# Kernel tuning notes

Measured on AMD Instinct MI355X. Metric: run time of the kernel, lower is better.

## Reference

```python
import jax, jax.numpy as jnp
import numpy as np

N_HEAD = 16
N_KV_HEAD = 4
N_EMBD = 2048
HEAD_DIM = N_EMBD // N_HEAD  # 128
RMS_EPS = float(np.finfo(np.float32).eps)  # torch F.rms_norm default eps


def _apply_rotary(x, cos, sin):
    # x: [B,T,H,D]; cos/sin: [1,T,1,D/2]
    d = x.shape[-1] // 2
    x1, x2 = x[..., :d], x[..., d:]
    y1 = x1 * cos + x2 * sin
    y2 = -x1 * sin + x2 * cos
    return jnp.concatenate([y1, y2], axis=-1)


def _rms_norm(x):
    var = jnp.mean(jnp.square(x), axis=-1, keepdims=True)
    return x * jax.lax.rsqrt(var + RMS_EPS)


def setup_inputs() -> dict:
    key = jax.random.key(0)
    ks = jax.random.split(key, 7)
    B, T = 2, 2048
    x = jax.random.normal(ks[0], (B, T, N_EMBD), dtype=jnp.float32)
    cos = jax.random.normal(ks[1], (1, T, 1, HEAD_DIM // 2), dtype=jnp.float32)
    sin = jax.random.normal(ks[2], (1, T, 1, HEAD_DIM // 2), dtype=jnp.float32)
    s = 1.0 / np.sqrt(N_EMBD)
    Wq = jax.random.normal(ks[3], (N_HEAD * HEAD_DIM, N_EMBD), dtype=jnp.float32) * s
    Wk = jax.random.normal(ks[4], (N_KV_HEAD * HEAD_DIM, N_EMBD), dtype=jnp.float32) * s
    Wv = jax.random.normal(ks[5], (N_KV_HEAD * HEAD_DIM, N_EMBD), dtype=jnp.float32) * s
    Wo = jax.random.normal(ks[6], (N_EMBD, N_EMBD), dtype=jnp.float32) * s
    return {"x": x, "cos": cos, "sin": sin, "Wq": Wq, "Wk": Wk, "Wv": Wv, "Wo": Wo}


def reference(x, cos, sin, Wq, Wk, Wv, Wo):
    B, T, C = x.shape
    q = (x @ Wq.T).reshape(B, T, N_HEAD, HEAD_DIM)
    k = (x @ Wk.T).reshape(B, T, N_KV_HEAD, HEAD_DIM)
    v = (x @ Wv.T).reshape(B, T, N_KV_HEAD, HEAD_DIM)
    q = _rms_norm(_apply_rotary(q, cos, sin))
    k = _rms_norm(_apply_rotary(k, cos, sin))
    # to [B,H,T,D]; expand kv heads for GQA
    q = q.transpose(0, 2, 1, 3)
    k = k.transpose(0, 2, 1, 3)
    v = v.transpose(0, 2, 1, 3)
    g = N_HEAD // N_KV_HEAD
    k = jnp.repeat(k, g, axis=1)
    v = jnp.repeat(v, g, axis=1)
    scale = 1.0 / np.sqrt(HEAD_DIM)
    scores = jnp.einsum("bhtd,bhsd->bhts", q, k) * scale
    causal = jnp.tril(jnp.ones((T, T), dtype=bool))
    scores = jnp.where(causal, scores, -jnp.inf)
    attn = jax.nn.softmax(scores, axis=-1)
    y = jnp.einsum("bhts,bhsd->bhtd", attn, v)
    y = y.transpose(0, 2, 1, 3).reshape(B, T, C)
    return y @ Wo.T
```

## Files before the change

kernel.cpp:

```cpp
#include <hip/hip_runtime.h>
#include <hip/hip_bf16.h>
#include <stdint.h>

#define B_   2
#define T_   2048
#define CEMB 2048
#define H_   16
#define HKV_ 4
#define D_   128

typedef __attribute__((ext_vector_type(8))) short bf16x8;
typedef __attribute__((ext_vector_type(4))) float f32x4;
typedef __attribute__((ext_vector_type(16))) float f32x16;

#if __has_builtin(__builtin_amdgcn_exp2f)
#define EXP2(x) __builtin_amdgcn_exp2f(x)
#else
#define EXP2(x) exp2f(x)
#endif

__device__ __forceinline__ unsigned short f2b(float f) {
  union { float f; unsigned u; } v; v.f = f;
  unsigned r = v.u + 0x7FFFu + ((v.u >> 16) & 1u);
  return (unsigned short)(r >> 16);
}
__device__ __forceinline__ float b2f(unsigned short u) {
  union { unsigned u; float f; } v; v.u = ((unsigned)u) << 16; return v.f;
}
__device__ __forceinline__ unsigned cvtpk(float lo, float hi) {
  unsigned r;
  asm("v_cvt_pk_bf16_f32 %0, %1, %2" : "=v"(r) : "v"(lo), "v"(hi));
  return r;
}

#if __has_builtin(__builtin_amdgcn_permlane32_swap)
__device__ __forceinline__ void pl32(unsigned& a, unsigned& b) {
  auto r = __builtin_amdgcn_permlane32_swap(a, b, false, false);
  a = r[0]; b = r[1];
}
#else
__device__ __forceinline__ void pl32(unsigned& a, unsigned& b) {
  const bool hih = (threadIdx.x & 32) != 0;
  unsigned sa = __shfl_xor(a, 32), sb = __shfl_xor(b, 32);
  unsigned na = hih ? sb : a;
  unsigned nb = hih ? b : sa;
  a = na; b = nb;
}
#endif

__device__ __forceinline__ void gl16(const void* g, void* l) {
  __builtin_amdgcn_global_load_lds(
      (const __attribute__((address_space(1))) unsigned int*)g,
      (__attribute__((address_space(3))) unsigned int*)l, 16, 0, 0);
}

#define FENCE() asm volatile("" ::: "memory")

__global__ void cvt_kernel(const float* __restrict__ src,
                           unsigned short* __restrict__ dst, int n4) {
  int i = blockIdx.x * blockDim.x + threadIdx.x;
  const int stride = gridDim.x * blockDim.x;
  for (; i < n4; i += stride) {
    float4 v = ((const float4*)src)[i];
    ushort4 o;
    o.x = f2b(v.x); o.y = f2b(v.y); o.z = f2b(v.z); o.w = f2b(v.w);
    ((ushort4*)dst)[i] = o;
  }
}

__global__ __launch_bounds__(512, 2)
void gemm_n192(const unsigned short* __restrict__ A,
               const unsigned short* __restrict__ W,
               unsigned short* __restrict__ Cmat, int M, int N, int K) {
  __shared__ alignas(16) unsigned short As[2][2][128][64];
  __shared__ alignas(16) unsigned short Bs[2][192][64];

  const int tid  = threadIdx.x;
  const int lane = tid & 63;
  const int w    = tid >> 6;
  const int wr   = w >> 2;
  const int wc   = w & 3;
  const int l16  = lane & 15, g4 = lane >> 4;
  const int srow = lane >> 3;
  const int schk = lane & 7;

  const int gx  = gridDim.x;
  const int nwg = gx * gridDim.y;
  const int lin = blockIdx.y * gx + blockIdx.x;
  const int cpx = nwg >> 3;
  const int swz = (lin & 7) * cpx + (lin >> 3);
  const int m0 = (swz / gx) * 256;
  const int n0 = (swz % gx) * 192;

  const unsigned short* Ap = A + (size_t)m0 * K;
  const unsigned short* Wp = W + (size_t)n0 * K;
  const int nk = K >> 6;

  f32x4 acc[8][3] = {};

  auto stA = [&](int ts, int h) {
    const unsigned short* g = Ap + (size_t)(h * 128 + w * 8 + srow) * K
                                 + ts * 64 + ((schk ^ srow) << 3);
    unsigned short* l = &As[ts & 1][h][w * 8][0];
    gl16(g, l);
    gl16(g + (size_t)64 * K, l + 64 * 64);
  };
  auto stB = [&](int ts, int j) {
    const unsigned short* g = Wp + (size_t)(j * 64 + w * 8 + srow) * K
                                 + ts * 64 + ((schk ^ srow) << 3);
    gl16(g, &Bs[ts & 1][j * 64 + w * 8][0]);
  };

  stA(0, 0); stA(0, 1); stB(0, 0); stB(0, 1); stB(0, 2);
  stA(1, 0); stB(1, 0); stB(1, 1); stB(1, 2);
  asm volatile("s_waitcnt vmcnt(5)" ::: "memory");
  __builtin_amdgcn_s_barrier();
  FENCE();

  for (int t = 0; t < nk; ++t) {
    const int buf = t & 1;
    bf16x8 af[4][2], bfr[3][2];
    #pragma unroll
    for (int mi = 0; mi < 4; ++mi) {
      const int har = (mi * 2 + wr) * 16 + l16;
      #pragma unroll
      for (int ks = 0; ks < 2; ++ks)
        af[mi][ks] = *(const bf16x8*)&As[buf][0][har][((ks * 4 + g4) ^ (l16 & 7)) << 3];
    }
    #pragma unroll
    for (int fc = 0; fc < 3; ++fc) {
      const int br = wc * 48 + fc * 16 + l16;
      #pragma unroll
      for (int ks = 0; ks < 2; ++ks)
        bfr[fc][ks] = *(const bf16x8*)&Bs[buf][br][((ks * 4 + g4) ^ (l16 & 7)) << 3];
    }
    if (t + 1 < nk) stA(t + 1, 1);
    __builtin_amdgcn_s_setprio(1);
    #pragma unroll
    for (int mi = 0; mi < 4; ++mi) {
      #pragma unroll
      for (int fc = 0; fc < 3; ++fc) {
        f32x4 a = acc[mi][fc];
        a = __builtin_amdgcn_mfma_f32_16x16x32_bf16(af[mi][0], bfr[fc][0], a, 0, 0, 0);
        a = __builtin_amdgcn_mfma_f32_16x16x32_bf16(af[mi][1], bfr[fc][1], a, 0, 0, 0);
        acc[mi][fc] = a;
      }
    }
    __builtin_amdgcn_s_setprio(0);
    if (t + 2 < nk) asm volatile("s_waitcnt vmcnt(7)" ::: "memory");
    else            asm volatile("s_waitcnt vmcnt(0)" ::: "memory");
    __builtin_amdgcn_s_barrier();
    FENCE();
    #pragma unroll
    for (int mi = 0; mi < 4; ++mi) {
      const int har = (mi * 2 + wr) * 16 + l16;
      #pragma unroll
      for (int ks = 0; ks < 2; ++ks)
        af[mi][ks] = *(const bf16x8*)&As[buf][1][har][((ks * 4 + g4) ^ (l16 & 7)) << 3];
    }
    if (t + 2 < nk) { stA(t + 2, 0); stB(t + 2, 0); stB(t + 2, 1); stB(t + 2, 2); }
    __builtin_amdgcn_s_setprio(1);
    #pragma unroll
    for (int mi = 0; mi < 4; ++mi) {
      #pragma unroll
      for (int fc = 0; fc < 3; ++fc) {
        f32x4 a = acc[4 + mi][fc];
        a = __builtin_amdgcn_mfma_f32_16x16x32_bf16(af[mi][0], bfr[fc][0], a, 0, 0, 0);
        a = __builtin_amdgcn_mfma_f32_16x16x32_bf16(af[mi][1], bfr[fc][1], a, 0, 0, 0);
        acc[4 + mi][fc] = a;
      }
    }
    __builtin_amdgcn_s_setprio(0);
    if (t + 2 < nk) asm volatile("s_waitcnt vmcnt(7)" ::: "memory");
    else            asm volatile("s_waitcnt vmcnt(0)" ::: "memory");
    __builtin_amdgcn_s_barrier();
    FENCE();
  }

  #pragma unroll
  for (int fr = 0; fr < 8; ++fr) {
    const int hh = fr >> 2, mi = fr & 3;
    #pragma unroll
    for (int fc = 0; fc < 3; ++fc) {
      const int row = m0 + hh * 128 + (mi * 2 + wr) * 16 + g4 * 4;
      const int col = n0 + wc * 48 + fc * 16 + l16;
      #pragma unroll
      for (int r = 0; r < 4; ++r)
        Cmat[(size_t)(row + r) * N + col] = f2b(acc[fr][fc][r]);
    }
  }
}

__global__ __launch_bounds__(512, 2)
void gemm_n128(const unsigned short* __restrict__ A,
               const unsigned short* __restrict__ W,
               float* __restrict__ Cmat, int M, int N, int K) {
  __shared__ alignas(16) unsigned short As[2][2][128][64];
  __shared__ alignas(16) unsigned short Bs[2][2][64][64];

  const int tid  = threadIdx.x;
  const int lane = tid & 63;
  const int w    = tid >> 6;
  const int wr   = w >> 2;
  const int wc   = w & 3;
  const int l16  = lane & 15, g4 = lane >> 4;
  const int srow = lane >> 3;
  const int schk = lane & 7;

  const int gx  = gridDim.x;
  const int nwg = gx * gridDim.y;
  const int lin = blockIdx.y * gx + blockIdx.x;
  const int cpx = nwg >> 3;
  const int swz = (lin & 7) * cpx + (lin >> 3);
  const int m0 = (swz / gx) * 256;
  const int n0 = (swz % gx) * 128;

  const unsigned short* Ap = A + (size_t)m0 * K;
  const unsigned short* Wp = W + (size_t)n0 * K;
  const int nk = K >> 6;

  const int bh_ = wc >> 1;
  const int br0 = (wc & 1) * 32;

  f32x4 acc[8][2] = {};

  auto stA = [&](int ts, int h) {
    const unsigned short* g = Ap + (size_t)(h * 128 + w * 8 + srow) * K
                                 + ts * 64 + ((schk ^ srow) << 3);
    unsigned short* l = &As[ts & 1][h][w * 8][0];
    gl16(g, l);
    gl16(g + (size_t)64 * K, l + 64 * 64);
  };
  auto stB = [&](int ts, int h) {
    const unsigned short* g = Wp + (size_t)(h * 64 + w * 8 + srow) * K
                                 + ts * 64 + ((schk ^ srow) << 3);
    gl16(g, &Bs[ts & 1][h][w * 8][0]);
  };

  stA(0, 0); stA(0, 1); stB(0, 0); stB(0, 1);
  stA(1, 0); stB(1, 0); stB(1, 1);
  asm volatile("s_waitcnt vmcnt(4)" ::: "memory");
  __builtin_amdgcn_s_barrier();
  FENCE();

  for (int t = 0; t < nk; ++t) {
    const int buf = t & 1;
    bf16x8 af[4][2], bfr[2][2];
    #pragma unroll
    for (int mi = 0; mi < 4; ++mi) {
      const int har = (mi * 2 + wr) * 16 + l16;
      #pragma unroll
      for (int ks = 0; ks < 2; ++ks)
        af[mi][ks] = *(const bf16x8*)&As[buf][0][har][((ks * 4 + g4) ^ (l16 & 7)) << 3];
    }
    #pragma unroll
    for (int fc = 0; fc < 2; ++fc) {
      const int br = br0 + fc * 16 + l16;
      #pragma unroll
      for (int ks = 0; ks < 2; ++ks)
        bfr[fc][ks] = *(const bf16x8*)&Bs[buf][bh_][br][((ks * 4 + g4) ^ (l16 & 7)) << 3];
    }
    if (t + 1 < nk) stA(t + 1, 1);
    __builtin_amdgcn_s_setprio(1);
    #pragma unroll
    for (int mi = 0; mi < 4; ++mi) {
      #pragma unroll
      for (int fc = 0; fc < 2; ++fc) {
        f32x4 a = acc[mi][fc];
        a = __builtin_amdgcn_mfma_f32_16x16x32_bf16(af[mi][0], bfr[fc][0], a, 0, 0, 0);
        a = __builtin_amdgcn_mfma_f32_16x16x32_bf16(af[mi][1], bfr[fc][1], a, 0, 0, 0);
        acc[mi][fc] = a;
      }
    }
    __builtin_amdgcn_s_setprio(0);
    if (t + 2 < nk) asm volatile("s_waitcnt vmcnt(6)" ::: "memory");
    else            asm volatile("s_waitcnt vmcnt(0)" ::: "memory");
    __builtin_amdgcn_s_barrier();
    FENCE();
    #pragma unroll
    for (int mi = 0; mi < 4; ++mi) {
      const int har = (mi * 2 + wr) * 16 + l16;
      #pragma unroll
      for (int ks = 0; ks < 2; ++ks)
        af[mi][ks] = *(const bf16x8*)&As[buf][1][har][((ks * 4 + g4) ^ (l16 & 7)) << 3];
    }
    if (t + 2 < nk) { stA(t + 2, 0); stB(t + 2, 0); stB(t + 2, 1); }
    __builtin_amdgcn_s_setprio(1);
    #pragma unroll
    for (int mi = 0; mi < 4; ++mi) {
      #pragma unroll
      for (int fc = 0; fc < 2; ++fc) {
        f32x4 a = acc[4 + mi][fc];
        a = __builtin_amdgcn_mfma_f32_16x16x32_bf16(af[mi][0], bfr[fc][0], a, 0, 0, 0);
        a = __builtin_amdgcn_mfma_f32_16x16x32_bf16(af[mi][1], bfr[fc][1], a, 0, 0, 0);
        acc[4 + mi][fc] = a;
      }
    }
    __builtin_amdgcn_s_setprio(0);
    if (t + 2 < nk) asm volatile("s_waitcnt vmcnt(6)" ::: "memory");
    else            asm volatile("s_waitcnt vmcnt(0)" ::: "memory");
    __builtin_amdgcn_s_barrier();
    FENCE();
  }

  #pragma unroll
  for (int fr = 0; fr < 8; ++fr) {
    const int hh = fr >> 2, mi = fr & 3;
    #pragma unroll
    for (int fc = 0; fc < 2; ++fc) {
      const int row = m0 + hh * 128 + (mi * 2 + wr) * 16 + g4 * 4;
      const int col = n0 + wc * 32 + fc * 16 + l16;
      #pragma unroll
      for (int r = 0; r < 4; ++r)
        Cmat[(size_t)(row + r) * N + col] = acc[fr][fc][r];
    }
  }
}

__global__ __launch_bounds__(128)
void rope_norm(const unsigned short* __restrict__ X, int rstride,
               const float* __restrict__ Cos, const float* __restrict__ Sin,
               unsigned short* __restrict__ Out, int Hn, float out_scale) {
  const int idx = blockIdx.x;
  const int h  = idx % Hn;
  const int bt = idx / Hn;
  const int t  = bt & (T_ - 1);
  const int b  = bt >> 11;
  const int d  = threadIdx.x;
  const unsigned short* src = X + (size_t)bt * rstride + h * D_;
  float y;
  if (d < 64) {
    float x1 = b2f(src[d]), x2 = b2f(src[d + 64]);
    float c = Cos[t * 64 + d], s = Sin[t * 64 + d];
    y = x1 * c + x2 * s;
  } else {
    int dd = d - 64;
    float x1 = b2f(src[dd]), x2 = b2f(src[d]);
    float c = Cos[t * 64 + dd], s = Sin[t * 64 + dd];
    y = -x1 * s + x2 * c;
  }
  float ss = y * y;
  #pragma unroll
  for (int m = 32; m; m >>= 1) ss += __shfl_xor(ss, m);
  __shared__ float red[2];
  if ((d & 63) == 0) red[d >> 6] = ss;
  __syncthreads();
  const float tot  = red[0] + red[1];
  const float rinv = rsqrtf(tot * (1.0f / 128.0f) + 1.1920929e-7f) * out_scale;
  Out[(((size_t)b * Hn + h) * T_ + t) * D_ + d] = f2b(y * rinv);
}

__global__ __launch_bounds__(256)
void vtrans(const unsigned short* __restrict__ Vf, int rstride,
            unsigned short* __restrict__ Vt) {
  __shared__ float tile[32][65];
  const int t0 = blockIdx.x * 64;
  const int d0 = blockIdx.y * 32;
  const int bh = blockIdx.z;
  const int b = bh >> 2, hk = bh & 3;
  const int tid = threadIdx.x;
  {
    const int di = tid & 31, ts = tid >> 5;
    #pragma unroll
    for (int i = 0; i < 8; ++i) {
      int tt = ts + i * 8;
      tile[di][tt] = b2f(Vf[(size_t)(b * T_ + t0 + tt) * rstride + hk * D_ + d0 + di]);
    }
  }
  __syncthreads();
  {
    const int ti = tid & 63, ds = tid >> 6;
    #pragma unroll
    for (int i = 0; i < 8; ++i) {
      int dd = ds * 8 + i;
      Vt[((size_t)bh * D_ + d0 + dd) * T_ + t0 + ti] = f2b(tile[dd][ti]);
    }
  }
}

#define KVB 128

__global__ __launch_bounds__(512)
void attn_kernel(const unsigned short* __restrict__ Qn,
                 const unsigned short* __restrict__ Kn,
                 const unsigned short* __restrict__ Vt,
                 unsigned short* __restrict__ Yb) {
  __shared__ alignas(16) unsigned short Ks[2][KVB][D_];
  __shared__ alignas(16) unsigned short Vs[2][D_][KVB];

  const int tid = threadIdx.x;
  const int lane = tid & 63;
  const int w = tid >> 6;
  const int wq  = w & 3;
  const int kvg = w >> 2;
  const int l31 = lane & 31;
  const int hi  = lane >> 5;
  const int bh = blockIdx.x;
  const int by = blockIdx.y;
  const int qt = (by < 8) ? by : 23 - by;
  const int b = bh >> 4, h = bh & 15;
  const int hk = h >> 2;

  const unsigned short* kp = Kn + ((size_t)(b * HKV_ + hk) * T_) * D_;
  const unsigned short* vp = Vt + ((size_t)(b * HKV_ + hk) * D_) * T_;

  const int r4 = lane >> 4, c16 = lane & 15;

  const int t0 = qt * 128;
  const int qrow0 = t0 + wq * 32;
  const int qmax = qrow0 + 31;
  const int nt = qt + 1;
  const int qglob = qrow0 + l31;

  const unsigned short* qp = Qn + ((size_t)bh * T_ + qrow0) * D_;
  bf16x8 qf[8];
  #pragma unroll
  for (int ds = 0; ds < 8; ++ds)
    qf[ds] = *(const bf16x8*)(qp + (size_t)l31 * D_ + ds * 16 + hi * 8);

  f32x16 o[4] = {};
  float l_lane = 0.f;

  auto stage = [&](int tt) {
    const int buf = tt & 1;
    const int kv = tt * KVB;
    #pragma unroll
    for (int j = 0; j < 4; ++j) {
      const int row = w * 16 + j * 4 + r4;
      const int cg = c16 ^ (row & 7);
      gl16(kp + (size_t)(kv + row) * D_ + cg * 8, &Ks[buf][w * 16 + j * 4][0]);
    }
    #pragma unroll
    for (int j = 0; j < 4; ++j) {
      const int row = w * 16 + j * 4 + r4;
      const int cg = c16 ^ (row & 7);
      gl16(vp + (size_t)row * T_ + kv + cg * 8, &Vs[buf][w * 16 + j * 4][0]);
    }
  };

  stage(0);

  union PAu { unsigned u[4]; bf16x8 v; };

  for (int t = 0; t < nt; ++t) {
    __syncthreads();
    if (t + 1 < nt) stage(t + 1);
    const int kbase = t * KVB + kvg * 64;
    if (kbase <= qmax) {
      const unsigned short (*kb)[D_]  = Ks[t & 1];
      const unsigned short (*vbp)[KVB] = Vs[t & 1];
      f32x16 s0 = {}, s1 = {};
      __builtin_amdgcn_s_setprio(1);
      #pragma unroll
      for (int ds = 0; ds < 8; ++ds) {
        const int key0 = kvg * 64 + l31;
        const int key1 = kvg * 64 + 32 + l31;
        bf16x8 k0 = *(const bf16x8*)&kb[key0][(((ds * 2 + hi) ^ (key0 & 7)) << 3)];
        bf16x8 k1 = *(const bf16x8*)&kb[key1][(((ds * 2 + hi) ^ (key1 & 7)) << 3)];
        s0 = __builtin_amdgcn_mfma_f32_32x32x16_bf16(k0, qf[ds], s0, 0, 0, 0);
        s1 = __builtin_amdgcn_mfma_f32_32x32x16_bf16(k1, qf[ds], s1, 0, 0, 0);
      }
      __builtin_amdgcn_s_setprio(0);
      const bool need_mask = (kbase + 63 > qrow0);
      float e0[16], e1[16];
      float ls = 0.f;
      #pragma unroll
      for (int r = 0; r < 16; ++r) {
        const int crow = (r & 3) + 8 * (r >> 2) + 4 * hi;
        float v0 = EXP2(s0[r]);
        float v1 = EXP2(s1[r]);
        if (need_mask) {
          v0 = (kbase + crow      <= qglob) ? v0 : 0.f;
          v1 = (kbase + 32 + crow <= qglob) ? v1 : 0.f;
        }
        e0[r] = v0; e1[r] = v1;
        ls += v0 + v1;
      }
      l_lane += ls;
      PAu pa[4];
      {
        unsigned a0 = cvtpk(e0[0],  e0[1]),  a1 = cvtpk(e0[2],  e0[3]);
        unsigned b0 = cvtpk(e0[4],  e0[5]),  b1 = cvtpk(e0[6],  e0[7]);
        unsigned c0 = cvtpk(e0[8],  e0[9]),  c1 = cvtpk(e0[10], e0[11]);
        unsigned d0 = cvtpk(e0[12], e0[13]), d1 = cvtpk(e0[14], e0[15]);
        pl32(a0, b0); pl32(a1, b1); pl32(c0, d0); pl32(c1, d1);
        pa[0].u[0] = a0; pa[0].u[1] = a1; pa[0].u[2] = b0; pa[0].u[3] = b1;
        pa[1].u[0] = c0; pa[1].u[1] = c1; pa[1].u[2] = d0; pa[1].u[3] = d1;
      }
      {
        unsigned a0 = cvtpk(e1[0],  e1[1]),  a1 = cvtpk(e1[2],  e1[3]);
        unsigned b0 = cvtpk(e1[4],  e1[5]),  b1 = cvtpk(e1[6],  e1[7]);
        unsigned c0 = cvtpk(e1[8],  e1[9]),  c1 = cvtpk(e1[10], e1[11]);
        unsigned d0 = cvtpk(e1[12], e1[13]), d1 = cvtpk(e1[14], e1[15]);
        pl32(a0, b0); pl32(a1, b1); pl32(c0, d0); pl32(c1, d1);
        pa[2].u[0] = a0; pa[2].u[1] = a1; pa[2].u[2] = b0; pa[2].u[3] = b1;
        pa[3].u[0] = c0; pa[3].u[1] = c1; pa[3].u[2] = d0; pa[3].u[3] = d1;
      }
      __builtin_amdgcn_s_setprio(1);
      #pragma unroll
      for (int ks = 0; ks < 4; ++ks) {
        #pragma unroll
        for (int db = 0; db < 4; ++db) {
          const int d = db * 32 + l31;
          const int c = (kvg * 8 + ks * 2 + hi) ^ (d & 7);
          bf16x8 vf = *(const bf16x8*)&vbp[d][c << 3];
          o[db] = __builtin_amdgcn_mfma_f32_32x32x16_bf16(pa[ks].v, vf, o[db], 0, 0, 0);
        }
      }
      __builtin_amdgcn_s_setprio(0);
    }
  }

  const float lfull = l_lane + __shfl_xor(l_lane, 32);
  __syncthreads();
  float* obuf = (float*)&Ks[0][0][0];
  float* lbuf = (float*)&Vs[0][0][0];
  if (w >= 4) {
    const int base = (w - 4) * 4096;
    #pragma unroll
    for (int r = 0; r < 16; ++r)
      #pragma unroll
      for (int db = 0; db < 4; ++db)
        obuf[base + (r * 4 + db) * 64 + lane] = o[db][r];
    if (hi == 0) lbuf[(w - 4) * 32 + l31] = lfull;
  }
  __syncthreads();
  if (w < 4) {
    const int base = w * 4096;
    const float ltot = lfull + lbuf[w * 32 + l31];
    const float invq = 1.0f / ltot;
    #pragma unroll
    for (int r = 0; r < 16; ++r) {
      const int crow = (r & 3) + 8 * (r >> 2) + 4 * hi;
      const float inv = __shfl(invq, crow);
      unsigned short* yrow = Yb + ((size_t)(b * T_ + qrow0 + crow) * CEMB) + h * D_;
      #pragma unroll
      for (int db = 0; db < 4; ++db)
        yrow[db * 32 + l31] = f2b((o[db][r] + obuf[base + (r * 4 + db) * 64 + lane]) * inv);
    }
  }
}

extern "C" void kernel_launch(void* const* d_in, const int* in_sizes, int n_in,
                              void* d_out, int out_size, void* d_ws, size_t ws_size,
                              hipStream_t stream) {
  const float* x    = (const float*)d_in[0];
  const float* cosp = (const float*)d_in[1];
  const float* sinp = (const float*)d_in[2];
  const float* Wq   = (const float*)d_in[3];
  const float* Wk   = (const float*)d_in[4];
  const float* Wv   = (const float*)d_in[5];
  const float* Wo   = (const float*)d_in[6];
  float* out = (float*)d_out;

  char* ws = (char*)d_ws;
  size_t off = 0;
  auto alloc = [&](size_t bytes) {
    void* p = ws + off;
    off += (bytes + 255) & ~(size_t)255;
    return p;
  };
  const size_t MT = (size_t)B_ * T_;
  const int NQKV = 3072;
  unsigned short* xb    = (unsigned short*)alloc(MT * CEMB * 2);
  unsigned short* wqkvb = (unsigned short*)alloc((size_t)NQKV * 2048 * 2);
  unsigned short* wob   = (unsigned short*)alloc((size_t)2048 * 2048 * 2);
  unsigned short* qkvb  = (unsigned short*)alloc(MT * NQKV * 2);
  unsigned short* qn    = (unsigned short*)alloc((size_t)B_ * H_ * T_ * D_ * 2);
  unsigned short* kn    = (unsigned short*)alloc((size_t)B_ * HKV_ * T_ * D_ * 2);
  unsigned short* vt    = (unsigned short*)alloc((size_t)B_ * HKV_ * D_ * T_ * 2);
  unsigned short* yb    = (unsigned short*)alloc(MT * CEMB * 2);

  cvt_kernel<<<2048, 256, 0, stream>>>(x,  xb, (int)(MT * CEMB / 4));
  cvt_kernel<<<1024, 256, 0, stream>>>(Wq, wqkvb,                2048 * 2048 / 4);
  cvt_kernel<<<256,  256, 0, stream>>>(Wk, wqkvb + 2048 * 2048,  512 * 2048 / 4);
  cvt_kernel<<<256,  256, 0, stream>>>(Wv, wqkvb + 2560 * 2048,  512 * 2048 / 4);
  cvt_kernel<<<1024, 256, 0, stream>>>(Wo, wob,                  2048 * 2048 / 4);

  gemm_n192<<<dim3(NQKV / 192, 4096 / 256), 512, 0, stream>>>(xb, wqkvb, qkvb, 4096, NQKV, 2048);

  rope_norm<<<4096 * H_,   128, 0, stream>>>(qkvb,        NQKV, cosp, sinp, qn, H_,   0.1275174324f);
  rope_norm<<<4096 * HKV_, 128, 0, stream>>>(qkvb + 2048, NQKV, cosp, sinp, kn, HKV_, 1.0f);
  vtrans<<<dim3(T_ / 64, D_ / 32, B_ * HKV_), 256, 0, stream>>>(qkvb + 2560, NQKV, vt);

  attn_kernel<<<dim3(B_ * H_, 16), 512, 0, stream>>>(qn, kn, vt, yb);

  gemm_n128<<<dim3(2048 / 128, 4096 / 256), 512, 0, stream>>>(yb, wob, out, 4096, 2048, 2048);
}
```

Baseline: 197.1 us.

## Retile GEMM warps to 4x2 grid, simplify pipeline, widen attention LDS swizzle

Both GEMM kernels change their wave layout from 2x4 to 4x2. Each wave now covers a 64-row by 96- or 64-column sub-tile and runs a single half-step per K-tile instead of two halves. This cuts per-wave LDS fragment loads for A, but the K-tile prefetch now issues all loads for the next stage at once and waits with vmcnt(0) every iteration, which may expose memory latency. The attention kernel's K/V shared-memory XOR swizzle widens from 8 to 16 chunks to reduce bank conflicts on the 128-wide rows.

Result: no change. 195.6 us (-0.7%).

```diff
diff --git a/kernel.cpp b/kernel.cpp
--- a/kernel.cpp
+++ b/kernel.cpp
@@ -78,8 +78,8 @@
   const int tid  = threadIdx.x;
   const int lane = tid & 63;
   const int w    = tid >> 6;
-  const int wr   = w >> 2;
-  const int wc   = w & 3;
+  const int wm   = w >> 1;
+  const int wn   = w & 1;
   const int l16  = lane & 15, g4 = lane >> 4;
   const int srow = lane >> 3;
   const int schk = lane & 7;
@@ -96,7 +96,10 @@
   const unsigned short* Wp = W + (size_t)n0 * K;
   const int nk = K >> 6;
 
-  f32x4 acc[8][3] = {};
+  const int hA  = wm >> 1;
+  const int ra0 = (wm & 1) * 64;
+
+  f32x4 acc[4][6] = {};
 
   auto stA = [&](int ts, int h) {
     const unsigned short* g = Ap + (size_t)(h * 128 + w * 8 + srow) * K
@@ -112,34 +115,36 @@
   };
 
   stA(0, 0); stA(0, 1); stB(0, 0); stB(0, 1); stB(0, 2);
-  stA(1, 0); stB(1, 0); stB(1, 1); stB(1, 2);
-  asm volatile("s_waitcnt vmcnt(5)" ::: "memory");
+  asm volatile("s_waitcnt vmcnt(0)" ::: "memory");
   __builtin_amdgcn_s_barrier();
   FENCE();
 
   for (int t = 0; t < nk; ++t) {
     const int buf = t & 1;
-    bf16x8 af[4][2], bfr[3][2];
+    bf16x8 af[4][2], bfr[6][2];
     #pragma unroll
     for (int mi = 0; mi < 4; ++mi) {
-      const int har = (mi * 2 + wr) * 16 + l16;
+      const int ar = ra0 + mi * 16 + l16;
       #pragma unroll
       for (int ks = 0; ks < 2; ++ks)
-        af[mi][ks] = *(const bf16x8*)&As[buf][0][har][((ks * 4 + g4) ^ (l16 & 7)) << 3];
-    }
-    #pragma unroll
-    for (int fc = 0; fc < 3; ++fc) {
-      const int br = wc * 48 + fc * 16 + l16;
+        af[mi][ks] = *(const bf16x8*)&As[buf][hA][ar][((ks * 4 + g4) ^ (l16 & 7)) << 3];
+    }
+    #pragma unroll
+    for (int fc = 0; fc < 6; ++fc) {
+      const int br = wn * 96 + fc * 16 + l16;
       #pragma unroll
       for (int ks = 0; ks < 2; ++ks)
         bfr[fc][ks] = *(const bf16x8*)&Bs[buf][br][((ks * 4 + g4) ^ (l16 & 7)) << 3];
     }
-    if (t + 1 < nk) stA(t + 1, 1);
+    if (t + 1 < nk) {
+      stA(t + 1, 0); stA(t + 1, 1);
+      stB(t + 1, 0); stB(t + 1, 1); stB(t + 1, 2);
+    }
     __builtin_amdgcn_s_setprio(1);
     #pragma unroll
     for (int mi = 0; mi < 4; ++mi) {
       #pragma unroll
-      for (int fc = 0; fc < 3; ++fc) {
+      for (int fc = 0; fc < 6; ++fc) {
         f32x4 a = acc[mi][fc];
         a = __builtin_amdgcn_mfma_f32_16x16x32_bf16(af[mi][0], bfr[fc][0], a, 0, 0, 0);
         a = __builtin_amdgcn_mfma_f32_16x16x32_bf16(af[mi][1], bfr[fc][1], a, 0, 0, 0);
@@ -147,46 +152,20 @@
       }
     }
     __builtin_amdgcn_s_setprio(0);
-    if (t + 2 < nk) asm volatile("s_waitcnt vmcnt(7)" ::: "memory");
-    else            asm volatile("s_waitcnt vmcnt(0)" ::: "memory");
+    asm volatile("s_waitcnt vmcnt(0)" ::: "memory");
     __builtin_amdgcn_s_barrier();
     FENCE();
-    #pragma unroll
-    for (int mi = 0; mi < 4; ++mi) {
-      const int har = (mi * 2 + wr) * 16 + l16;
-      #pragma unroll
-      for (int ks = 0; ks < 2; ++ks)
-        af[mi][ks] = *(const bf16x8*)&As[buf][1][har][((ks * 4 + g4) ^ (l16 & 7)) << 3];
-    }
-    if (t + 2 < nk) { stA(t + 2, 0); stB(t + 2, 0); stB(t + 2, 1); stB(t + 2, 2); }
-    __builtin_amdgcn_s_setprio(1);
-    #pragma unroll
-    for (int mi = 0; mi < 4; ++mi) {
-      #pragma unroll
-      for (int fc = 0; fc < 3; ++fc) {
-        f32x4 a = acc[4 + mi][fc];
-        a = __builtin_amdgcn_mfma_f32_16x16x32_bf16(af[mi][0], bfr[fc][0], a, 0, 0, 0);
-        a = __builtin_amdgcn_mfma_f32_16x16x32_bf16(af[mi][1], bfr[fc][1], a, 0, 0, 0);
-        acc[4 + mi][fc] = a;
-      }
-    }
-    __builtin_amdgcn_s_setprio(0);
-    if (t + 2 < nk) asm volatile("s_waitcnt vmcnt(7)" ::: "memory");
-    else            asm volatile("s_waitcnt vmcnt(0)" ::: "memory");
-    __builtin_amdgcn_s_barrier();
-    FENCE();
   }
 
   #pragma unroll
-  for (int fr = 0; fr < 8; ++fr) {
-    const int hh = fr >> 2, mi = fr & 3;
-    #pragma unroll
-    for (int fc = 0; fc < 3; ++fc) {
-      const int row = m0 + hh * 128 + (mi * 2 + wr) * 16 + g4 * 4;
-      const int col = n0 + wc * 48 + fc * 16 + l16;
+  for (int mi = 0; mi < 4; ++mi) {
+    #pragma unroll
+    for (int fc = 0; fc < 6; ++fc) {
+      const int row = m0 + wm * 64 + mi * 16 + g4 * 4;
+      const int col = n0 + wn * 96 + fc * 16 + l16;
       #pragma unroll
       for (int r = 0; r < 4; ++r)
-        Cmat[(size_t)(row + r) * N + col] = f2b(acc[fr][fc][r]);
+        Cmat[(size_t)(row + r) * N + col] = f2b(acc[mi][fc][r]);
     }
   }
 }
@@ -201,8 +180,8 @@
   const int tid  = threadIdx.x;
   const int lane = tid & 63;
   const int w    = tid >> 6;
-  const int wr   = w >> 2;
-  const int wc   = w & 3;
+  const int wm   = w >> 1;
+  const int wn   = w & 1;
   const int l16  = lane & 15, g4 = lane >> 4;
   const int srow = lane >> 3;
   const int schk = lane & 7;
@@ -219,10 +198,10 @@
   const unsigned short* Wp = W + (size_t)n0 * K;
   const int nk = K >> 6;
 
-  const int bh_ = wc >> 1;
-  const int br0 = (wc & 1) * 32;
-
-  f32x4 acc[8][2] = {};
+  const int hA  = wm >> 1;
+  const int ra0 = (wm & 1) * 64;
+
+  f32x4 acc[4][4] = {};
 
   auto stA = [&](int ts, int h) {
     const unsigned short* g = Ap + (size_t)(h * 128 + w * 8 + srow) * K
@@ -238,34 +217,37 @@
   };
 
   stA(0, 0); stA(0, 1); stB(0, 0); stB(0, 1);
-  stA(1, 0); stB(1, 0); stB(1, 1);
-  asm volatile("s_waitcnt vmcnt(4)" ::: "memory");
+  asm volatile("s_waitcnt vmcnt(0)" ::: "memory");
   __builtin_amdgcn_s_barrier();
   FENCE();
 
   for (int t = 0; t < nk; ++t) {
     const int buf = t & 1;
-    bf16x8 af[4][2], bfr[2][2];
+    bf16x8 af[4][2], bfr[4][2];
     #pragma unroll
     for (int mi = 0; mi < 4; ++mi) {
-      const int har = (mi * 2 + wr) * 16 + l16;
+      const int ar = ra0 + mi * 16 + l16;
       #pragma unroll
       for (int ks = 0; ks < 2; ++ks)
-        af[mi][ks] = *(const bf16x8*)&As[buf][0][har][((ks * 4 + g4) ^ (l16 & 7)) << 3];
-    }
-    #pragma unroll
-    for (int fc = 0; fc < 2; ++fc) {
-      const int br = br0 + fc * 16 + l16;
+        af[mi][ks] = *(const bf16x8*)&As[buf][hA][ar][((ks * 4 + g4) ^ (l16 & 7)) << 3];
+    }
+    #pragma unroll
+    for (int fc = 0; fc < 4; ++fc) {
+      const int br = wn * 64 + fc * 16 + l16;
+      const int hb = br >> 6, rb = br & 63;
       #pragma unroll
       for (int ks = 0; ks < 2; ++ks)
-        bfr[fc][ks] = *(const bf16x8*)&Bs[buf][bh_][br][((ks * 4 + g4) ^ (l16 & 7)) << 3];
-    }
-    if (t + 1 < nk) stA(t + 1, 1);
+        bfr[fc][ks] = *(const bf16x8*)&Bs[buf][hb][rb][((ks * 4 + g4) ^ (l16 & 7)) << 3];
+    }
+    if (t + 1 < nk) {
+      stA(t + 1, 0); stA(t + 1, 1);
+      stB(t + 1, 0); stB(t + 1, 1);
+    }
     __builtin_amdgcn_s_setprio(1);
     #pragma unroll
     for (int mi = 0; mi < 4; ++mi) {
       #pragma unroll
-      for (int fc = 0; fc < 2; ++fc) {
+      for (int fc = 0; fc < 4; ++fc) {
         f32x4 a = acc[mi][fc];
         a = __builtin_amdgcn_mfma_f32_16x16x32_bf16(af[mi][0], bfr[fc][0], a, 0, 0, 0);
         a = __builtin_amdgcn_mfma_f32_16x16x32_bf16(af[mi][1], bfr[fc][1], a, 0, 0, 0);
@@ -273,46 +255,20 @@
       }
     }
     __builtin_amdgcn_s_setprio(0);
-    if (t + 2 < nk) asm volatile("s_waitcnt vmcnt(6)" ::: "memory");
-    else            asm volatile("s_waitcnt vmcnt(0)" ::: "memory");
+    asm volatile("s_waitcnt vmcnt(0)" ::: "memory");
     __builtin_amdgcn_s_barrier();
     FENCE();
-    #pragma unroll
-    for (int mi = 0; mi < 4; ++mi) {
-      const int har = (mi * 2 + wr) * 16 + l16;
-      #pragma unroll
-      for (int ks = 0; ks < 2; ++ks)
-        af[mi][ks] = *(const bf16x8*)&As[buf][1][har][((ks * 4 + g4) ^ (l16 & 7)) << 3];
-    }
-    if (t + 2 < nk) { stA(t + 2, 0); stB(t + 2, 0); stB(t + 2, 1); }
-    __builtin_amdgcn_s_setprio(1);
-    #pragma unroll
-    for (int mi = 0; mi < 4; ++mi) {
-      #pragma unroll
-      for (int fc = 0; fc < 2; ++fc) {
-        f32x4 a = acc[4 + mi][fc];
-        a = __builtin_amdgcn_mfma_f32_16x16x32_bf16(af[mi][0], bfr[fc][0], a, 0, 0, 0);
-        a = __builtin_amdgcn_mfma_f32_16x16x32_bf16(af[mi][1], bfr[fc][1], a, 0, 0, 0);
-        acc[4 + mi][fc] = a;
-      }
-    }
-    __builtin_amdgcn_s_setprio(0);
-    if (t + 2 < nk) asm volatile("s_waitcnt vmcnt(6)" ::: "memory");
-    else            asm volatile("s_waitcnt vmcnt(0)" ::: "memory");
-    __builtin_amdgcn_s_barrier();
-    FENCE();
   }
 
   #pragma unroll
-  for (int fr = 0; fr < 8; ++fr) {
-    const int hh = fr >> 2, mi = fr & 3;
-    #pragma unroll
-    for (int fc = 0; fc < 2; ++fc) {
-      const int row = m0 + hh * 128 + (mi * 2 + wr) * 16 + g4 * 4;
-      const int col = n0 + wc * 32 + fc * 16 + l16;
+  for (int mi = 0; mi < 4; ++mi) {
+    #pragma unroll
+    for (int fc = 0; fc < 4; ++fc) {
+      const int row = m0 + wm * 64 + mi * 16 + g4 * 4;
+      const int col = n0 + wn * 64 + fc * 16 + l16;
       #pragma unroll
       for (int r = 0; r < 4; ++r)
-        Cmat[(size_t)(row + r) * N + col] = acc[fr][fc][r];
+        Cmat[(size_t)(row + r) * N + col] = acc[mi][fc][r];
     }
   }
 }
@@ -427,13 +383,13 @@
     #pragma unroll
     for (int j = 0; j < 4; ++j) {
       const int row = w * 16 + j * 4 + r4;
-      const int cg = c16 ^ (row & 7);
+      const int cg = c16 ^ (row & 15);
       gl16(kp + (size_t)(kv + row) * D_ + cg * 8, &Ks[buf][w * 16 + j * 4][0]);
     }
     #pragma unroll
     for (int j = 0; j < 4; ++j) {
       const int row = w * 16 + j * 4 + r4;
-      const int cg = c16 ^ (row & 7);
+      const int cg = c16 ^ (row & 15);
       gl16(vp + (size_t)row * T_ + kv + cg * 8, &Vs[buf][w * 16 + j * 4][0]);
     }
   };
@@ -455,8 +411,8 @@
       for (int ds = 0; ds < 8; ++ds) {
         const int key0 = kvg * 64 + l31;
         const int key1 = kvg * 64 + 32 + l31;
-        bf16x8 k0 = *(const bf16x8*)&kb[key0][(((ds * 2 + hi) ^ (key0 & 7)) << 3)];
-        bf16x8 k1 = *(const bf16x8*)&kb[key1][(((ds * 2 + hi) ^ (key1 & 7)) << 3)];
+        bf16x8 k0 = *(const bf16x8*)&kb[key0][(((ds * 2 + hi) ^ (key0 & 15)) << 3)];
+        bf16x8 k1 = *(const bf16x8*)&kb[key1][(((ds * 2 + hi) ^ (key1 & 15)) << 3)];
         s0 = __builtin_amdgcn_mfma_f32_32x32x16_bf16(k0, qf[ds], s0, 0, 0, 0);
         s1 = __builtin_amdgcn_mfma_f32_32x32x16_bf16(k1, qf[ds], s1, 0, 0, 0);
       }
@@ -502,7 +458,7 @@
         #pragma unroll
         for (int db = 0; db < 4; ++db) {
           const int d = db * 32 + l31;
-          const int c = (kvg * 8 + ks * 2 + hi) ^ (d & 7);
+          const int c = (kvg * 8 + ks * 2 + hi) ^ (d & 15);
           bf16x8 vf = *(const bf16x8*)&vbp[d][c << 3];
           o[db] = __builtin_amdgcn_mfma_f32_32x32x16_bf16(pa[ks].v, vf, o[db], 0, 0, 0);
         }
```
